# Performance work log

Hardware: AMD Instinct MI355X
Metric: run time of the kernel (lower is better)

## Reference

```python
import jax, jax.numpy as jnp
import numpy as np

B = 2048
IN_DIM = 8192
OUT_DIM = 16384
N_GATES = 16


def setup_inputs() -> dict:
    key = jax.random.key(0)
    k1, k2, k3, k4 = jax.random.split(key, 4)
    x = jax.random.uniform(k1, (B, IN_DIM), dtype=jnp.float32)  # values in [0,1]
    logits = jax.random.normal(k2, (OUT_DIM, N_GATES), dtype=jnp.float32)  # init_std=1.0
    # fixed random connectivity: permutation trick from _pairwise_random_connections
    perm = jax.random.permutation(k3, 2 * OUT_DIM) % IN_DIM
    perm = jax.random.permutation(k4, IN_DIM)[perm]
    c = perm.reshape(2, OUT_DIM)
    return {
        "x": x,
        "logits": logits,
        "a_idx": c[0].astype(jnp.int32),
        "b_idx": c[1].astype(jnp.int32),
    }


def _bin_op_s(a, b, p):
    # a, b: (B, out_dim); p: (out_dim, 16) gate probabilities, broadcast over batch.
    # Weighted sum of the 16 real-valued relaxations of 2-input Boolean gates
    # (standard DiffLogic gate ordering; gate 0 is constant 0, gate 15 constant 1).
    ab = a * b
    return (
        p[:, 1] * ab                          # AND
        + p[:, 2] * (a - ab)                  # a AND NOT b
        + p[:, 3] * a                         # a
        + p[:, 4] * (b - ab)                  # NOT a AND b
        + p[:, 5] * b                         # b
        + p[:, 6] * (a + b - 2.0 * ab)        # XOR
        + p[:, 7] * (a + b - ab)              # OR
        + p[:, 8] * (1.0 - (a + b - ab))      # NOR
        + p[:, 9] * (1.0 - (a + b - 2.0 * ab))  # XNOR
        + p[:, 10] * (1.0 - b)                # NOT b
        + p[:, 11] * (1.0 - b + ab)           # a OR NOT b
        + p[:, 12] * (1.0 - a)                # NOT a
        + p[:, 13] * (1.0 - a + ab)           # NOT a OR b
        + p[:, 14] * (1.0 - ab)               # NAND
        + p[:, 15]                            # constant 1
    )


def reference(x, logits, a_idx, b_idx):
    # Gather the two inputs of each output gate: (B, out_dim)
    a = x[:, a_idx]
    b = x[:, b_idx]
    # Training mode: softmax relaxation over the 16 gates per node.
    p = jax.nn.softmax(logits, axis=-1)
    return _bin_op_s(a, b, p)
```

## Files before the change

### kernel.cpp

```cpp
#include <hip/hip_runtime.h>
#include <hip/hip_bf16.h>

#define IN_DIM  8192
#define OUT_DIM 16384
#define BATCH   2048
#define NG      16
#define RROWS   2
#define TPB     512
#define NITER   (OUT_DIM / 4 / TPB)

typedef float        f32x2 __attribute__((ext_vector_type(2)));
typedef float        f32x4 __attribute__((ext_vector_type(4)));
typedef unsigned int u32x4 __attribute__((ext_vector_type(4)));


__device__ __forceinline__ void collapse_weights(const float* __restrict__ l,
                                                 float& w_ab, float& w_a,
                                                 float& w_b, float& w_c) {
    float v[NG];
    float m = -1e30f;
#pragma unroll
    for (int k = 0; k < NG; ++k) { v[k] = l[k]; m = fmaxf(m, v[k]); }
    float s = 0.f;
#pragma unroll
    for (int k = 0; k < NG; ++k) { v[k] = __expf(v[k] - m); s += v[k]; }
    float inv = 1.0f / s;
#pragma unroll
    for (int k = 0; k < NG; ++k) v[k] *= inv;
    w_ab = v[1] - v[2] - v[4] - 2.f * v[6] - v[7] + v[8] + 2.f * v[9]
         + v[11] + v[13] - v[14];
    w_a  = v[2] + v[3] + v[6] + v[7] - v[8] - v[9] - v[12] - v[13];
    w_b  = v[4] + v[5] + v[6] + v[7] - v[8] - v[9] - v[10] - v[11];
    w_c  = v[8] + v[9] + v[10] + v[11] + v[12] + v[13] + v[14] + v[15];
}

__global__ __launch_bounds__(256) void gate_weights_kernel(
    const float* __restrict__ logits,
    const int* __restrict__ a_idx, const int* __restrict__ b_idx,
    float* __restrict__ ws) {
    int j = blockIdx.x * blockDim.x + threadIdx.x;
    if (j >= OUT_DIM) return;
    float w_ab, w_a, w_b, w_c;
    collapse_weights(logits + (size_t)j * NG, w_ab, w_a, w_b, w_c);
    ws[j]               = w_ab;
    ws[j +     OUT_DIM] = w_a;
    ws[j + 2 * OUT_DIM] = w_b;
    ws[j + 3 * OUT_DIM] = w_c;
    unsigned int* pk = (unsigned int*)(ws + 4 * OUT_DIM);
    pk[j] = (unsigned int)a_idx[j] | ((unsigned int)b_idx[j] << 16);
}

__global__ __launch_bounds__(TPB, 4) void gate_eval_kernel(
    const float* __restrict__ x,
    const float* __restrict__ ws,
    f32x4* __restrict__ out4) {
    __shared__ f32x2 rows2[IN_DIM];
    const int i0 = blockIdx.x * RROWS;

    const f32x4* wab4 = (const f32x4*)(ws);
    const f32x4* wa4  = (const f32x4*)(ws + OUT_DIM);
    const f32x4* wb4  = (const f32x4*)(ws + 2 * OUT_DIM);
    const f32x4* wc4  = (const f32x4*)(ws + 3 * OUT_DIM);
    const u32x4* pk4  = (const u32x4*)(ws + 4 * OUT_DIM);

    u32x4 pkb[2];
    f32x4 wabb[2], wab_[2], wbb[2], wcb[2];
    {
        int j4 = threadIdx.x;
        pkb[0]  = pk4[j4];
        wabb[0] = wab4[j4];
        wab_[0] = wa4[j4];
        wbb[0]  = wb4[j4];
        wcb[0]  = wc4[j4];
    }

    const f32x4* xr0 = (const f32x4*)(x + (size_t)i0 * IN_DIM);
    const f32x4* xr1 = (const f32x4*)(x + (size_t)(i0 + 1) * IN_DIM);
#pragma unroll
    for (int t = 0; t < IN_DIM / 4 / TPB; ++t) {
        int m = threadIdx.x + t * TPB;
        f32x4 r0 = xr0[m];
        f32x4 r1 = xr1[m];
#pragma unroll
        for (int c = 0; c < 4; ++c) {
            f32x2 p; p.x = r0[c]; p.y = r1[c];
            rows2[m * 4 + c] = p;
        }
    }
    __syncthreads();

    f32x4* o0 = out4 + (size_t)i0 * (OUT_DIM / 4);
    f32x4* o1 = o0 + (OUT_DIM / 4);

#pragma unroll
    for (int k = 0; k < NITER; ++k) {
        const int cur = k & 1, nxt = cur ^ 1;
        if (k + 1 < NITER) {
            int j4n = threadIdx.x + (k + 1) * TPB;
            pkb[nxt]  = pk4[j4n];
            wabb[nxt] = wab4[j4n];
            wab_[nxt] = wa4[j4n];
            wbb[nxt]  = wb4[j4n];
            wcb[nxt]  = wc4[j4n];
        }
        int j4 = threadIdx.x + k * TPB;
        u32x4 pk = pkb[cur];
        f32x4 wab = wabb[cur], wa = wab_[cur], wb = wbb[cur], wc = wcb[cur];
        f32x4 r0, r1;
#pragma unroll
        for (int c = 0; c < 4; ++c) {
            f32x2 va = rows2[pk[c] & 0xFFFFu];
            f32x2 vb = rows2[pk[c] >> 16];
            r0[c] = fmaf(wab[c], va.x * vb.x,
                         fmaf(wa[c], va.x, fmaf(wb[c], vb.x, wc[c])));
            r1[c] = fmaf(wab[c], va.y * vb.y,
                         fmaf(wa[c], va.y, fmaf(wb[c], vb.y, wc[c])));
        }
        __builtin_nontemporal_store(r0, &o0[j4]);
        __builtin_nontemporal_store(r1, &o1[j4]);
    }
}

__global__ __launch_bounds__(256) void gate_eval_fused_kernel(
    const float* __restrict__ x,
    const float* __restrict__ logits,
    const int* __restrict__ a_idx,
    const int* __restrict__ b_idx,
    float* __restrict__ out) {
    __shared__ float row[IN_DIM];
    const int i = blockIdx.x;
    const f32x4* xr = (const f32x4*)(x + (size_t)i * IN_DIM);
    f32x4* rv = (f32x4*)row;
#pragma unroll
    for (int t = 0; t < IN_DIM / 4 / 256; ++t)
        rv[threadIdx.x + t * 256] = xr[threadIdx.x + t * 256];
    __syncthreads();
    float* o = out + (size_t)i * OUT_DIM;
    for (int k = 0; k < OUT_DIM / 256; ++k) {
        int j = threadIdx.x + k * 256;
        float w_ab, w_a, w_b, w_c;
        collapse_weights(logits + (size_t)j * NG, w_ab, w_a, w_b, w_c);
        float a = row[a_idx[j]], b = row[b_idx[j]];
        o[j] = fmaf(w_ab, a * b, fmaf(w_a, a, fmaf(w_b, b, w_c)));
    }
}

extern "C" void kernel_launch(void* const* d_in, const int* in_sizes, int n_in,
                              void* d_out, int out_size, void* d_ws, size_t ws_size,
                              hipStream_t stream) {
    const float* x      = (const float*)d_in[0];
    const float* logits = (const float*)d_in[1];
    const int*   a_idx  = (const int*)d_in[2];
    const int*   b_idx  = (const int*)d_in[3];
    float* out = (float*)d_out;

    const size_t ws_need = (size_t)(4 * OUT_DIM) * sizeof(float)
                         + (size_t)OUT_DIM * sizeof(unsigned int);
    if (ws_size >= ws_need && d_ws != nullptr) {
        float* ws = (float*)d_ws;
        gate_weights_kernel<<<OUT_DIM / 256, 256, 0, stream>>>(
            logits, a_idx, b_idx, ws);
        gate_eval_kernel<<<BATCH / RROWS, TPB, 0, stream>>>(
            x, ws, (f32x4*)out);
    } else {
        gate_eval_fused_kernel<<<BATCH, 256, 0, stream>>>(
            x, logits, a_idx, b_idx, out);
    }
}
```

Before: 40.03 us.

## Pack row pairs as bf16 in LDS and prefetch next row pair during compute

Each block now handles two row pairs, one from each half of the batch. The rows are stored in shared memory as packed bf16 pairs, which halves LDS use. While the first pair is being evaluated, the second pair's x rows are loaded and packed into a second buffer, overlapping global loads with gather compute. Grid size is halved. Rounding inputs to bf16 lowers accuracy, and the output may drift past tolerance.

After: 40.94 us. 2.3% more time.

```diff
diff --git a/kernel.cpp b/kernel.cpp
--- a/kernel.cpp
+++ b/kernel.cpp
@@ -6,10 +6,11 @@
 #define BATCH   2048
 #define NG      16
 #define RROWS   2
+#define GROUPS  2
 #define TPB     512
+#define NBLK    (BATCH / RROWS / GROUPS)
 #define NITER   (OUT_DIM / 4 / TPB)
 
-typedef float        f32x2 __attribute__((ext_vector_type(2)));
 typedef float        f32x4 __attribute__((ext_vector_type(4)));
 typedef unsigned int u32x4 __attribute__((ext_vector_type(4)));
 
@@ -50,12 +51,26 @@
     pk[j] = (unsigned int)a_idx[j] | ((unsigned int)b_idx[j] << 16);
 }
 
+__device__ __forceinline__ float bf16_hi_to_f(unsigned int u) {
+    union { unsigned int i; float f; } c; c.i = u & 0xFFFF0000u; return c.f;
+}
+__device__ __forceinline__ float bf16_lo_to_f(unsigned int u) {
+    union { unsigned int i; float f; } c; c.i = u << 16; return c.f;
+}
+__device__ __forceinline__ unsigned int pack2(float a, float b) {
+    return (unsigned int)__bfloat16_as_ushort(__float2bfloat16(a))
+         | ((unsigned int)__bfloat16_as_ushort(__float2bfloat16(b)) << 16);
+}
+
 __global__ __launch_bounds__(TPB, 4) void gate_eval_kernel(
     const float* __restrict__ x,
     const float* __restrict__ ws,
     f32x4* __restrict__ out4) {
-    __shared__ f32x2 rows2[IN_DIM];
-    const int i0 = blockIdx.x * RROWS;
+    __shared__ unsigned int buf0[IN_DIM];
+    __shared__ unsigned int buf1[IN_DIM];
+    const int b  = blockIdx.x;
+    const int i0 = RROWS * b;
+    const int i1 = RROWS * b + BATCH / GROUPS;
 
     const f32x4* wab4 = (const f32x4*)(ws);
     const f32x4* wa4  = (const f32x4*)(ws + OUT_DIM);
@@ -74,23 +89,63 @@
         wcb[0]  = wc4[j4];
     }
 
-    const f32x4* xr0 = (const f32x4*)(x + (size_t)i0 * IN_DIM);
-    const f32x4* xr1 = (const f32x4*)(x + (size_t)(i0 + 1) * IN_DIM);
-#pragma unroll
-    for (int t = 0; t < IN_DIM / 4 / TPB; ++t) {
-        int m = threadIdx.x + t * TPB;
-        f32x4 r0 = xr0[m];
-        f32x4 r1 = xr1[m];
+    const float* xA = x + (size_t)i0 * IN_DIM;
+#pragma unroll
+    for (int t = 0; t < IN_DIM / TPB; ++t) {
+        int k = threadIdx.x + t * TPB;
+        buf0[k] = pack2(xA[k], xA[k + IN_DIM]);
+    }
+    __syncthreads();
+
+    const float* xB = x + (size_t)i1 * IN_DIM;
+    f32x4* oA = out4 + (size_t)i0 * (OUT_DIM / 4);
+    f32x4* oB = out4 + (size_t)i1 * (OUT_DIM / 4);
+
+#pragma unroll
+    for (int k = 0; k < NITER; ++k) {
+        {
+            int ka = threadIdx.x + (2 * k) * TPB;
+            int kb = threadIdx.x + (2 * k + 1) * TPB;
+            unsigned int va = pack2(xB[ka], xB[ka + IN_DIM]);
+            unsigned int vb = pack2(xB[kb], xB[kb + IN_DIM]);
+            buf1[ka] = va;
+            buf1[kb] = vb;
+        }
+        const int cur = k & 1, nxt = cur ^ 1;
+        if (k + 1 < NITER) {
+            int j4n = threadIdx.x + (k + 1) * TPB;
+            pkb[nxt]  = pk4[j4n];
+            wabb[nxt] = wab4[j4n];
+            wab_[nxt] = wa4[j4n];
+            wbb[nxt]  = wb4[j4n];
+            wcb[nxt]  = wc4[j4n];
+        }
+        int j4 = threadIdx.x + k * TPB;
+        u32x4 pk = pkb[cur];
+        f32x4 wab = wabb[cur], wa = wab_[cur], wb = wbb[cur], wc = wcb[cur];
+        f32x4 r0, r1;
 #pragma unroll
         for (int c = 0; c < 4; ++c) {
-            f32x2 p; p.x = r0[c]; p.y = r1[c];
-            rows2[m * 4 + c] = p;
-        }
+            unsigned int va = buf0[pk[c] & 0xFFFFu];
+            unsigned int vb = buf0[pk[c] >> 16];
+            float a0 = bf16_lo_to_f(va), a1 = bf16_hi_to_f(va);
+            float b0 = bf16_lo_to_f(vb), b1 = bf16_hi_to_f(vb);
+            r0[c] = fmaf(wab[c], a0 * b0, fmaf(wa[c], a0, fmaf(wb[c], b0, wc[c])));
+            r1[c] = fmaf(wab[c], a1 * b1, fmaf(wa[c], a1, fmaf(wb[c], b1, wc[c])));
+        }
+        __builtin_nontemporal_store(r0, &oA[j4]);
+        __builtin_nontemporal_store(r1, &oA[j4 + OUT_DIM / 4]);
+    }
+
+    {
+        int j4 = threadIdx.x;
+        pkb[0]  = pk4[j4];
+        wabb[0] = wab4[j4];
+        wab_[0] = wa4[j4];
+        wbb[0]  = wb4[j4];
+        wcb[0]  = wc4[j4];
     }
     __syncthreads();
-
-    f32x4* o0 = out4 + (size_t)i0 * (OUT_DIM / 4);
-    f32x4* o1 = o0 + (OUT_DIM / 4);
 
 #pragma unroll
     for (int k = 0; k < NITER; ++k) {
@@ -109,15 +164,15 @@
         f32x4 r0, r1;
 #pragma unroll
         for (int c = 0; c < 4; ++c) {
-            f32x2 va = rows2[pk[c] & 0xFFFFu];
-            f32x2 vb = rows2[pk[c] >> 16];
-            r0[c] = fmaf(wab[c], va.x * vb.x,
-                         fmaf(wa[c], va.x, fmaf(wb[c], vb.x, wc[c])));
-            r1[c] = fmaf(wab[c], va.y * vb.y,
-                         fmaf(wa[c], va.y, fmaf(wb[c], vb.y, wc[c])));
-        }
-        __builtin_nontemporal_store(r0, &o0[j4]);
-        __builtin_nontemporal_store(r1, &o1[j4]);
+            unsigned int va = buf1[pk[c] & 0xFFFFu];
+            unsigned int vb = buf1[pk[c] >> 16];
+            float a0 = bf16_lo_to_f(va), a1 = bf16_hi_to_f(va);
+            float b0 = bf16_lo_to_f(vb), b1 = bf16_hi_to_f(vb);
+            r0[c] = fmaf(wab[c], a0 * b0, fmaf(wa[c], a0, fmaf(wb[c], b0, wc[c])));
+            r1[c] = fmaf(wab[c], a1 * b1, fmaf(wa[c], a1, fmaf(wb[c], b1, wc[c])));
+        }
+        __builtin_nontemporal_store(r0, &oB[j4]);
+        __builtin_nontemporal_store(r1, &oB[j4 + OUT_DIM / 4]);
     }
 }
 
@@ -160,8 +215,7 @@
         float* ws = (float*)d_ws;
         gate_weights_kernel<<<OUT_DIM / 256, 256, 0, stream>>>(
             logits, a_idx, b_idx, ws);
-        gate_eval_kernel<<<BATCH / RROWS, TPB, 0, stream>>>(
-            x, ws, (f32x4*)out);
+        gate_eval_kernel<<<NBLK, TPB, 0, stream>>>(x, ws, (f32x4*)out);
     } else {
         gate_eval_fused_kernel<<<BATCH, 256, 0, stream>>>(
             x, logits, a_idx, b_idx, out);
```
